# Kernel tuning notes

Hardware: AMD Instinct MI355X
Metric: run time of the kernel (lower is better)

## Reference

```python
import jax, jax.numpy as jnp
import numpy as np

NUM_HEADS = 16

def setup_inputs() -> dict:
    key = jax.random.key(0)
    ks = jax.random.split(key, 7)
    B, N, D = 2, 2048, 1024
    x = jax.random.normal(ks[0], (B, N, D), dtype=jnp.float32)
    gamma = jax.random.uniform(ks[1], (B, NUM_HEADS), dtype=jnp.float32)
    dist_matrix = jax.random.uniform(ks[2], (N, N), dtype=jnp.float32)
    W_qkv = jax.random.normal(ks[3], (D, 3 * D), dtype=jnp.float32) * (D ** -0.5)
    b_qkv = jnp.zeros((3 * D,), dtype=jnp.float32)
    W_proj = jax.random.normal(ks[4], (D, D), dtype=jnp.float32) * (D ** -0.5)
    b_proj = jnp.zeros((D,), dtype=jnp.float32)
    return {"x": x, "gamma": gamma, "dist_matrix": dist_matrix,
            "W_qkv": W_qkv, "b_qkv": b_qkv, "W_proj": W_proj, "b_proj": b_proj}

def reference(x, gamma, dist_matrix, W_qkv, b_qkv, W_proj, b_proj):
    B, N, D = x.shape
    H = NUM_HEADS
    hd = D // H
    scale = D ** -0.5  # standard_scale=False -> dim**-0.5
    # qkv projection: [B,N,3D] -> [3,B,H,N,hd]
    qkv = (x @ W_qkv + b_qkv).reshape(B, N, 3, H, hd).transpose(2, 0, 3, 1, 4)
    q, k, v = qkv[0], qkv[1], qkv[2]
    # scores with zoom bias: [B,H,N,N]
    scores = jnp.einsum('bhnd,bhmd->bhnm', q, k) * scale
    scores = scores - gamma[:, :, None, None] * dist_matrix[None, None, :, :]
    attn = jax.nn.softmax(scores, axis=-1)
    out = jnp.einsum('bhnm,bhmd->bhnd', attn, v)  # [B,H,N,hd]
    out = out.transpose(0, 2, 1, 3).reshape(B, N, D)
    return out @ W_proj + b_proj
```

## Files before the change

kernel.cpp:

```cpp
#include <hip/hip_runtime.h>
#include <cstdint>
#include <cstddef>

#define HD 64
#define NH 16
#define BATCH 2
#define SEQ 2048
#define DIM 1024
#define SCALE 0.03125f
#define LOG2E 1.4426950408889634f
#define QSCALE (SCALE * LOG2E)
#define NT (SEQ / 64)
#define NT2 32
#define SOFF 16.0f

typedef short bf16x8 __attribute__((ext_vector_type(8)));
typedef float f32x4 __attribute__((ext_vector_type(4)));
typedef unsigned u32x2 __attribute__((ext_vector_type(2)));
typedef unsigned u32x4 __attribute__((ext_vector_type(4)));

#define GL16(gp, lp) __builtin_amdgcn_global_load_lds( \
    (const __attribute__((address_space(1))) unsigned int*)(gp), \
    (__attribute__((address_space(3))) unsigned int*)(lp), 16, 0, 0)

static __device__ __forceinline__ unsigned short f2bf(float f) {
  union { float f; unsigned u; } a; a.f = f;
  unsigned r = a.u + 0x7fffu + ((a.u >> 16) & 1u);
  return (unsigned short)(r >> 16);
}

static __device__ __forceinline__ f32x4 zero4() {
  f32x4 z; z[0] = 0.f; z[1] = 0.f; z[2] = 0.f; z[3] = 0.f; return z;
}

__global__ void convert_x(const float* __restrict__ in, unsigned short* __restrict__ out, int n4) {
  int i = blockIdx.x * blockDim.x + threadIdx.x;
  if (i < n4) {
    float4 v = reinterpret_cast<const float4*>(in)[i];
    ushort4 o;
    o.x = f2bf(v.x); o.y = f2bf(v.y); o.z = f2bf(v.z); o.w = f2bf(v.w);
    reinterpret_cast<ushort4*>(out)[i] = o;
  }
}

__global__ void transpose_convert(const float* __restrict__ in, unsigned short* __restrict__ out,
                                  int R, int C) {
  __shared__ float tile[32][33];
  int bx = blockIdx.x * 32;
  int by = blockIdx.y * 32;
  int tx = threadIdx.x, ty = threadIdx.y;
  #pragma unroll
  for (int i = 0; i < 32; i += 8)
    tile[ty + i][tx] = in[(size_t)(by + ty + i) * C + bx + tx];
  __syncthreads();
  #pragma unroll
  for (int i = 0; i < 32; i += 8)
    out[(size_t)(bx + ty + i) * R + by + tx] = f2bf(tile[tx][ty + i]);
}

__global__ __launch_bounds__(256) void gemm128(
    const unsigned short* __restrict__ A, const unsigned short* __restrict__ Bt,
    const float* __restrict__ bias, int K, int mode,
    unsigned short* __restrict__ qo, unsigned short* __restrict__ ko,
    unsigned short* __restrict__ vo, float* __restrict__ outf) {
  __shared__ __attribute__((aligned(16))) unsigned short As[128 * 64];
  __shared__ __attribute__((aligned(16))) unsigned short Bs[128 * 64];
  const int tid = threadIdx.x;
  const int lane = tid & 63, w = tid >> 6;
  const int lo = lane & 15, hi = lane >> 4;
  const int wm = w >> 1, wn = w & 1;
  const int gx = gridDim.x;
  const int nwg = gx * gridDim.y;
  const int flat = blockIdx.y * gx + blockIdx.x;
  const int swz = (flat & 7) * (nwg >> 3) + (flat >> 3);
  const int m0 = (swz / gx) * 128, n0 = (swz % gx) * 128;
  const int srow = tid >> 3, scol = (tid & 7) * 8;
  const unsigned short* abase = A + (size_t)(m0 + srow) * K + scol;
  const unsigned short* bbase = Bt + (size_t)(n0 + srow) * K + scol;

  f32x4 acc[4][4];
  #pragma unroll
  for (int mr = 0; mr < 4; ++mr)
    #pragma unroll
    for (int nr = 0; nr < 4; ++nr) acc[mr][nr] = zero4();

  const int nkt = K / 64;
  for (int kt = 0; kt < nkt; ++kt) {
    const unsigned short* ak = abase + kt * 64;
    const unsigned short* bk = bbase + kt * 64;
    #pragma unroll
    for (int i = 0; i < 4; ++i) {
      GL16(ak + (size_t)(32 * i) * K, &As[(w * 64 + 256 * i) * 8]);
      GL16(bk + (size_t)(32 * i) * K, &Bs[(w * 64 + 256 * i) * 8]);
    }
    __syncthreads();
    __builtin_amdgcn_s_setprio(1);
    #pragma unroll
    for (int kc = 0; kc < 2; ++kc) {
      bf16x8 af[4], bfr[4];
      #pragma unroll
      for (int mr = 0; mr < 4; ++mr)
        af[mr] = *reinterpret_cast<const bf16x8*>(
            &As[(wm * 64 + mr * 16 + lo) * 64 + kc * 32 + hi * 8]);
      #pragma unroll
      for (int nr = 0; nr < 4; ++nr)
        bfr[nr] = *reinterpret_cast<const bf16x8*>(
            &Bs[(wn * 64 + nr * 16 + lo) * 64 + kc * 32 + hi * 8]);
      #pragma unroll
      for (int mr = 0; mr < 4; ++mr)
        #pragma unroll
        for (int nr = 0; nr < 4; ++nr)
          acc[mr][nr] = __builtin_amdgcn_mfma_f32_16x16x32_bf16(af[mr], bfr[nr], acc[mr][nr], 0, 0, 0);
    }
    __builtin_amdgcn_s_setprio(0);
    __syncthreads();
  }

  #pragma unroll
  for (int nr = 0; nr < 4; ++nr) {
    const int gcol = n0 + wn * 64 + nr * 16 + lo;
    const float bv = bias[gcol];
    #pragma unroll
    for (int mr = 0; mr < 4; ++mr)
      #pragma unroll
      for (int j = 0; j < 4; ++j) {
        const int grow = m0 + wm * 64 + mr * 16 + hi * 4 + j;
        float val = acc[mr][nr][j] + bv;
        if (mode == 0) {
          int which = gcol >> 10;
          int hh = (gcol >> 6) & 15;
          int d = gcol & 63;
          int bb = grow >> 11;
          int n = grow & 2047;
          if (which == 0) {
            qo[((size_t)(bb * NH + hh) * SEQ + n) * HD + d] = f2bf(val * QSCALE);
          } else if (which == 1) {
            ko[((size_t)(bb * NH + hh) * SEQ + n) * HD + d] = f2bf(val);
          } else {
            vo[((size_t)(bb * NH + hh) * HD + d) * SEQ + n] = f2bf(val);
          }
        } else {
          outf[(size_t)grow * DIM + gcol] = val;
        }
      }
  }
}

__global__ __launch_bounds__(256, 6) void attn_split(
    const unsigned short* __restrict__ qb, const unsigned short* __restrict__ kb,
    const unsigned short* __restrict__ vtb, const float* __restrict__ gamma,
    const float* __restrict__ dist, float* __restrict__ oP, float* __restrict__ lP) {
  __shared__ __attribute__((aligned(16))) unsigned short Ks[2][32 * 64];
  __shared__ __attribute__((aligned(16))) unsigned short Vt[2][64 * 32];
  __shared__ __attribute__((aligned(16))) unsigned short Ps[4 * 16 * 32];
  const int tid = threadIdx.x;
  const int lane = tid & 63;
  const int w = tid >> 6;
  const int lo = lane & 15;
  const int hi = lane >> 4;
  const int idx = blockIdx.x;
  const int half = idx & 1;
  const int bh = (idx >> 1) & 31;
  const int qt = idx >> 6;
  const int qrow0 = qt * 64 + w * 16;
  const int kv0 = half * 1024;
  const float g2 = gamma[bh] * LOG2E;

  const size_t base = (size_t)bh * SEQ * HD;
  const size_t vtbase = (size_t)bh * HD * SEQ;

  bf16x8 qf[2];
  #pragma unroll
  for (int kc = 0; kc < 2; ++kc)
    qf[kc] = *reinterpret_cast<const bf16x8*>(
        &qb[base + (size_t)(qrow0 + lo) * HD + kc * 32 + hi * 8]);

  const float* drow = dist + (size_t)(qrow0 + lo) * SEQ + kv0 + hi * 4;

  f32x4 o[4];
  #pragma unroll
  for (int db = 0; db < 4; ++db) o[db] = zero4();
  float l_run = 0.f;

  const int ksr = tid >> 3;
  const int ksc = (tid & 7) ^ (ksr & 7);
  const unsigned short* ksrc = kb + base + (size_t)(kv0 + ksr) * HD + ksc * 8;
  const int vsr = tid >> 2;
  const int vsc = (tid & 3) ^ ((vsr >> 1) & 3);
  const unsigned short* vsrc = vtb + vtbase + (size_t)vsr * SEQ + kv0 + vsc * 8;

  unsigned short* const psw = &Ps[w * 512 + lo * 32];

  GL16(ksrc, &Ks[0][w * 512]);
  GL16(vsrc, &Vt[0][w * 512]);

#define SITER(T, CUR)                                                                  \
  {                                                                                    \
                                              \
    asm volatile("s_waitcnt vmcnt(1)" ::: "memory");                                   \
    __builtin_amdgcn_s_barrier();                                                      \
          \
    f32x4 dv[2];                                                                       \
    { const float* dp = drow + (T) * 32;                                               \
      dv[0] = *reinterpret_cast<const f32x4*>(dp);                                     \
      dv[1] = *reinterpret_cast<const f32x4*>(dp + 16);                                \
    }                                                                                  \
    __builtin_amdgcn_sched_barrier(0);                                                 \
    if ((T) + 1 < NT2) {                                                               \
      GL16(ksrc + (size_t)((T) + 1) * 32 * HD, &Ks[(CUR) ^ 1][w * 512]);               \
    }                                                                                  \
    __builtin_amdgcn_sched_barrier(0);                                                 \
                                                            \
    f32x4 s[2];                                                                        \
    s[0][0] = -SOFF; s[0][1] = -SOFF; s[0][2] = -SOFF; s[0][3] = -SOFF;                \
    s[1] = s[0];                                                                       \
    __builtin_amdgcn_s_setprio(1);                                                     \
    _Pragma("unroll")                                                                  \
    for (int nb = 0; nb < 2; ++nb)                                                     \
      _Pragma("unroll")                                                                \
      for (int kc = 0; kc < 2; ++kc) {                                                 \
        bf16x8 kf = *reinterpret_cast<const bf16x8*>(                                  \
            &Ks[CUR][(nb * 16 + lo) * 64 + ((kc * 4 + hi) ^ (lo & 7)) * 8]);           \
        s[nb] = __builtin_amdgcn_mfma_f32_16x16x32_bf16(kf, qf[kc], s[nb], 0, 0, 0);   \
      }                                                                                \
    __builtin_amdgcn_s_setprio(0);                                                     \
                \
    float psum = 0.f;                                                                  \
    _Pragma("unroll")                                                                  \
    for (int nb = 0; nb < 2; ++nb) {                                                   \
      float p0 = exp2f(__builtin_fmaf(-g2, dv[nb][0], s[nb][0]));                      \
      float p1 = exp2f(__builtin_fmaf(-g2, dv[nb][1], s[nb][1]));                      \
      float p2 = exp2f(__builtin_fmaf(-g2, dv[nb][2], s[nb][2]));                      \
      float p3 = exp2f(__builtin_fmaf(-g2, dv[nb][3], s[nb][3]));                      \
      psum += (p0 + p1) + (p2 + p3);                                                   \
      unsigned pk0, pk1;                                                               \
      asm("v_cvt_pk_bf16_f32 %0, %1, %2" : "=v"(pk0) : "v"(p0), "v"(p1));              \
      asm("v_cvt_pk_bf16_f32 %0, %1, %2" : "=v"(pk1) : "v"(p2), "v"(p3));              \
      u32x2 pw_; pw_[0] = pk0; pw_[1] = pk1;                                           \
      *reinterpret_cast<u32x2*>(&psw[((nb * 4 + hi) ^ (lo & 7)) * 4]) = pw_;           \
    }                                                                                  \
    psum += __shfl_xor(psum, 16, 64);                                                  \
    psum += __shfl_xor(psum, 32, 64);                                                  \
    l_run += psum;                                                                     \
                                  \
    if ((T) + 1 < NT2)                                                                 \
      asm volatile("s_waitcnt vmcnt(1)" ::: "memory");                                 \
    else                                                                               \
      asm volatile("s_waitcnt vmcnt(0)" ::: "memory");                                 \
    __builtin_amdgcn_s_barrier();                                                      \
    if ((T) + 1 < NT2) {                                                               \
      GL16(vsrc + ((T) + 1) * 32, &Vt[(CUR) ^ 1][w * 512]);                            \
    }                                                                                  \
    __builtin_amdgcn_sched_barrier(0);                                                 \
                                               \
    __builtin_amdgcn_s_setprio(1);                                                     \
    {                                                                                  \
      u32x2 ra = *reinterpret_cast<const u32x2*>(&psw[((hi * 2) ^ (lo & 7)) * 4]);     \
      u32x2 rb = *reinterpret_cast<const u32x2*>(&psw[((hi * 2 + 1) ^ (lo & 7)) * 4]); \
      u32x4 t_; t_[0] = ra[0]; t_[1] = ra[1]; t_[2] = rb[0]; t_[3] = rb[1];            \
      bf16x8 pf = __builtin_bit_cast(bf16x8, t_);                                      \
      _Pragma("unroll")                                                                \
      for (int db = 0; db < 4; ++db) {                                                 \
        bf16x8 vtf = *reinterpret_cast<const bf16x8*>(                                 \
            &Vt[CUR][(db * 16 + lo) * 32 + ((hi ^ ((lo >> 1) & 3))) * 8]);             \
        o[db] = __builtin_amdgcn_mfma_f32_16x16x32_bf16(vtf, pf, o[db], 0, 0, 0);      \
      }                                                                                \
    }                                                                                  \
    __builtin_amdgcn_s_setprio(0);                                                     \
  }

  for (int mt = 0; mt < NT2; mt += 2) {
    SITER(mt, 0)
    SITER(mt + 1, 1)
  }
#undef SITER

  {
    const size_t prow = (size_t)(half * 32 + bh) * SEQ + qrow0 + lo;
    float* op = oP + prow * HD + hi * 4;
    #pragma unroll
    for (int db = 0; db < 4; ++db)
      *reinterpret_cast<f32x4*>(op + db * 16) = o[db];
    if (hi == 0) lP[prow] = l_run;
  }
}

__global__ __launch_bounds__(256) void attn_combine(
    const float* __restrict__ oP, const float* __restrict__ lP,
    unsigned short* __restrict__ ab) {
  int g = blockIdx.x * blockDim.x + threadIdx.x;
  int row = g >> 4;
  int dc = (g & 15) * 4;
  int bh = row >> 11, n = row & 2047;
  int b = bh >> 4, h = bh & 15;
  f32x4 a = *reinterpret_cast<const f32x4*>(oP + (size_t)row * 64 + dc);
  f32x4 c = *reinterpret_cast<const f32x4*>(oP + 4194304 + (size_t)row * 64 + dc);
  float rl = 1.0f / (lP[row] + lP[65536 + row]);
  ushort4 w4;
  w4.x = f2bf((a[0] + c[0]) * rl);
  w4.y = f2bf((a[1] + c[1]) * rl);
  w4.z = f2bf((a[2] + c[2]) * rl);
  w4.w = f2bf((a[3] + c[3]) * rl);
  *reinterpret_cast<ushort4*>(&ab[((size_t)(b * SEQ + n)) * DIM + h * HD + dc]) = w4;
}

__global__ __launch_bounds__(256, 4) void attn_kernel(
    const unsigned short* __restrict__ qb, const unsigned short* __restrict__ kb,
    const unsigned short* __restrict__ vtb, const float* __restrict__ gamma,
    const float* __restrict__ dist, unsigned short* __restrict__ ab) {
  __shared__ __attribute__((aligned(16))) unsigned short Ks[2][64 * 64];
  __shared__ __attribute__((aligned(16))) unsigned short Vt[2][64 * 64];
  __shared__ __attribute__((aligned(16))) unsigned short Ps[4 * 16 * 64];
  const int tid = threadIdx.x;
  const int lane = tid & 63;
  const int w = tid >> 6;
  const int lo = lane & 15;
  const int hi = lane >> 4;
  const int idx = blockIdx.x;
  const int bh = idx & 31;
  const int qt = idx >> 5;
  const int b = bh >> 4, h = bh & 15;
  const int qrow0 = qt * 64 + w * 16;
  const float g2 = gamma[bh] * LOG2E;

  const size_t base = (size_t)bh * SEQ * HD;
  const size_t vtbase = (size_t)bh * HD * SEQ;

  bf16x8 qf[2];
  #pragma unroll
  for (int kc = 0; kc < 2; ++kc)
    qf[kc] = *reinterpret_cast<const bf16x8*>(
        &qb[base + (size_t)(qrow0 + lo) * HD + kc * 32 + hi * 8]);

  const float* drow = dist + (size_t)(qrow0 + lo) * SEQ + hi * 4;

  f32x4 o[4];
  #pragma unroll
  for (int db = 0; db < 4; ++db) o[db] = zero4();
  float l_run = 0.f;

  const int srow = tid >> 3;
  const int schunk = (tid & 7) ^ (srow & 7);
  const unsigned short* ksrc0 = kb + base + (size_t)srow * HD + schunk * 8;
  const unsigned short* ksrc1 = ksrc0 + (size_t)32 * HD;
  const unsigned short* vsrc0 = vtb + vtbase + (size_t)srow * SEQ + schunk * 8;
  const unsigned short* vsrc1 = vsrc0 + (size_t)32 * SEQ;

  unsigned short* const psw = &Ps[w * 1024 + lo * 64];

  GL16(ksrc0, &Ks[0][w * 512]);
  GL16(ksrc1, &Ks[0][2048 + w * 512]);
  GL16(vsrc0, &Vt[0][w * 512]);
  GL16(vsrc1, &Vt[0][2048 + w * 512]);

#define ITER(T, CUR)                                                                   \
  {                                                                                    \
    asm volatile("s_waitcnt vmcnt(2)" ::: "memory");                                   \
    __builtin_amdgcn_s_barrier();                                                      \
    f32x4 dv[4];                                                                       \
    { const float* dp = drow + (T) * 64;                                               \
      _Pragma("unroll")                                                                \
      for (int nb = 0; nb < 4; ++nb)                                                   \
        dv[nb] = *reinterpret_cast<const f32x4*>(dp + nb * 16);                        \
    }                                                                                  \
    __builtin_amdgcn_sched_barrier(0);                                                 \
    if ((T) + 1 < NT) {                                                                \
      const size_t m1 = (size_t)((T) + 1) * 64;                                        \
      GL16(ksrc0 + m1 * HD, &Ks[(CUR) ^ 1][w * 512]);                                  \
      GL16(ksrc1 + m1 * HD, &Ks[(CUR) ^ 1][2048 + w * 512]);                           \
    }                                                                                  \
    __builtin_amdgcn_sched_barrier(0);                                                 \
    f32x4 s[4];                                                                        \
    _Pragma("unroll")                                                                  \
    for (int nb = 0; nb < 4; ++nb) {                                                   \
      s[nb][0] = -SOFF; s[nb][1] = -SOFF; s[nb][2] = -SOFF; s[nb][3] = -SOFF;          \
    }                                                                                  \
    __builtin_amdgcn_s_setprio(1);                                                     \
    _Pragma("unroll")                                                                  \
    for (int nb = 0; nb < 4; ++nb)                                                     \
      _Pragma("unroll")                                                                \
      for (int kc = 0; kc < 2; ++kc) {                                                 \
        bf16x8 kf = *reinterpret_cast<const bf16x8*>(                                  \
            &Ks[CUR][(nb * 16 + lo) * 64 + ((kc * 4 + hi) ^ (lo & 7)) * 8]);           \
        s[nb] = __builtin_amdgcn_mfma_f32_16x16x32_bf16(kf, qf[kc], s[nb], 0, 0, 0);   \
      }                                                                                \
    __builtin_amdgcn_s_setprio(0);                                                     \
    float psum = 0.f;                                                                  \
    _Pragma("unroll")                                                                  \
    for (int nb = 0; nb < 4; ++nb) {                                                   \
      float p0 = exp2f(__builtin_fmaf(-g2, dv[nb][0], s[nb][0]));                      \
      float p1 = exp2f(__builtin_fmaf(-g2, dv[nb][1], s[nb][1]));                      \
      float p2 = exp2f(__builtin_fmaf(-g2, dv[nb][2], s[nb][2]));                      \
      float p3 = exp2f(__builtin_fmaf(-g2, dv[nb][3], s[nb][3]));                      \
      psum += (p0 + p1) + (p2 + p3);                                                   \
      unsigned pk0, pk1;                                                               \
      asm("v_cvt_pk_bf16_f32 %0, %1, %2" : "=v"(pk0) : "v"(p0), "v"(p1));              \
      asm("v_cvt_pk_bf16_f32 %0, %1, %2" : "=v"(pk1) : "v"(p2), "v"(p3));              \
      u32x2 pw_; pw_[0] = pk0; pw_[1] = pk1;                                           \
      *reinterpret_cast<u32x2*>(&psw[(((nb << 2) + hi) ^ lo) * 4]) = pw_;              \
    }                                                                                  \
    psum += __shfl_xor(psum, 16, 64);                                                  \
    psum += __shfl_xor(psum, 32, 64);                                                  \
    l_run += psum;                                                                     \
    if ((T) + 1 < NT)                                                                  \
      asm volatile("s_waitcnt vmcnt(2)" ::: "memory");                                 \
    else                                                                               \
      asm volatile("s_waitcnt vmcnt(0)" ::: "memory");                                 \
    __builtin_amdgcn_s_barrier();                                                      \
    if ((T) + 1 < NT) {                                                                \
      const int m1 = ((T) + 1) * 64;                                                   \
      GL16(vsrc0 + m1, &Vt[(CUR) ^ 1][w * 512]);                                       \
      GL16(vsrc1 + m1, &Vt[(CUR) ^ 1][2048 + w * 512]);                                \
    }                                                                                  \
    __builtin_amdgcn_sched_barrier(0);                                                 \
    __builtin_amdgcn_s_setprio(1);                                                     \
    _Pragma("unroll")                                                                  \
    for (int kc = 0; kc < 2; ++kc) {                                                   \
      u32x2 ra = *reinterpret_cast<const u32x2*>(&psw[(((kc << 3) + hi * 2) ^ lo) * 4]); \
      u32x2 rb = *reinterpret_cast<const u32x2*>(&psw[(((kc << 3) + hi * 2 + 1) ^ lo) * 4]); \
      u32x4 t_; t_[0] = ra[0]; t_[1] = ra[1]; t_[2] = rb[0]; t_[3] = rb[1];            \
      bf16x8 pf = __builtin_bit_cast(bf16x8, t_);                                      \
      _Pragma("unroll")                                                                \
      for (int db = 0; db < 4; ++db) {                                                 \
        bf16x8 vtf = *reinterpret_cast<const bf16x8*>(                                 \
            &Vt[CUR][(db * 16 + lo) * 64 + ((kc * 4 + hi) ^ (lo & 7)) * 8]);           \
        o[db] = __builtin_amdgcn_mfma_f32_16x16x32_bf16(vtf, pf, o[db], 0, 0, 0);      \
      }                                                                                \
    }                                                                                  \
    __builtin_amdgcn_s_setprio(0);                                                     \
  }

  for (int mt = 0; mt < NT; mt += 2) {
    ITER(mt, 0)
    ITER(mt + 1, 1)
  }
#undef ITER

  {
    float rl = 1.0f / l_run;
    size_t row = (size_t)b * SEQ + qrow0 + lo;
    #pragma unroll
    for (int db = 0; db < 4; ++db) {
      ushort4 w4;
      w4.x = f2bf(o[db][0] * rl);
      w4.y = f2bf(o[db][1] * rl);
      w4.z = f2bf(o[db][2] * rl);
      w4.w = f2bf(o[db][3] * rl);
      *reinterpret_cast<ushort4*>(&ab[row * DIM + h * HD + db * 16 + hi * 4]) = w4;
    }
  }
}

extern "C" void kernel_launch(void* const* d_in, const int* in_sizes, int n_in,
                              void* d_out, int out_size, void* d_ws, size_t ws_size,
                              hipStream_t stream) {
  const float* x     = (const float*)d_in[0];
  const float* gamma = (const float*)d_in[1];
  const float* dist  = (const float*)d_in[2];
  const float* Wqkv  = (const float*)d_in[3];
  const float* bqkv  = (const float*)d_in[4];
  const float* Wproj = (const float*)d_in[5];
  const float* bproj = (const float*)d_in[6];
  float* out = (float*)d_out;

  char* ws = (char*)d_ws;
  unsigned short* xb     = (unsigned short*)(ws);
  unsigned short* wqkvt  = (unsigned short*)(ws + 8388608);
  unsigned short* wprojt = (unsigned short*)(ws + 14680064);
  unsigned short* qbuf   = (unsigned short*)(ws + 16777216);
  unsigned short* kbuf   = (unsigned short*)(ws + 25165824);
  unsigned short* vtbuf  = (unsigned short*)(ws + 33554432);
  unsigned short* abuf   = (unsigned short*)(ws + 41943040);
  float* oP = (float*)(ws + 50331648);
  float* lP = (float*)(ws + 83886080);
  const bool split = ws_size >= (size_t)84410368;

  convert_x<<<4096, 256, 0, stream>>>(x, xb, (BATCH * SEQ * DIM) / 4);
  transpose_convert<<<dim3(96, 32), dim3(32, 8), 0, stream>>>(Wqkv, wqkvt, DIM, 3 * DIM);
  transpose_convert<<<dim3(32, 32), dim3(32, 8), 0, stream>>>(Wproj, wprojt, DIM, DIM);
  gemm128<<<dim3(24, 32), 256, 0, stream>>>(xb, wqkvt, bqkv, DIM, 0, qbuf, kbuf, vtbuf, nullptr);
  if (split) {
    attn_split<<<2048, 256, 0, stream>>>(qbuf, kbuf, vtbuf, gamma, dist, oP, lP);
    attn_combine<<<4096, 256, 0, stream>>>(oP, lP, abuf);
  } else {
    attn_kernel<<<(SEQ / 64) * BATCH * NH, 256, 0, stream>>>(qbuf, kbuf, vtbuf, gamma, dist, abuf);
  }
  gemm128<<<dim3(8, 32), 256, 0, stream>>>(abuf, wprojt, bproj, DIM, 1, nullptr, nullptr, nullptr, out);
}
```

Measured before the change: 192.5 us.

## Rework split attention to 32x32 MFMA tiles with register-level P transpose

Rewrites the split-KV attention kernel to use 32x32x16 bf16 MFMAs, with each wave owning 32 query rows and each block covering 128 query rows over 64-key tiles. The probability matrix is rearranged between the S and PV MFMAs with v_permlane32_swap in registers, replacing the previous round trip through an LDS scratch buffer. This cuts LDS traffic and per-MFMA overhead and halves the block count. The cost is higher register pressure (launch bounds lowered to 2), bigger K/V LDS tiles, and fewer blocks to spread across the CUs.

```diff
diff --git a/kernel.cpp b/kernel.cpp
--- a/kernel.cpp
+++ b/kernel.cpp
@@ -11,11 +11,12 @@
 #define LOG2E 1.4426950408889634f
 #define QSCALE (SCALE * LOG2E)
 #define NT (SEQ / 64)
-#define NT2 32
+#define NTH 16
 #define SOFF 16.0f
 
 typedef short bf16x8 __attribute__((ext_vector_type(8)));
 typedef float f32x4 __attribute__((ext_vector_type(4)));
+typedef float f32x16 __attribute__((ext_vector_type(16)));
 typedef unsigned u32x2 __attribute__((ext_vector_type(2)));
 typedef unsigned u32x4 __attribute__((ext_vector_type(4)));
 
@@ -146,142 +147,165 @@
   }
 }
 
-__global__ __launch_bounds__(256, 6) void attn_split(
+__global__ __launch_bounds__(256, 2) void attn_split2(
     const unsigned short* __restrict__ qb, const unsigned short* __restrict__ kb,
     const unsigned short* __restrict__ vtb, const float* __restrict__ gamma,
     const float* __restrict__ dist, float* __restrict__ oP, float* __restrict__ lP) {
-  __shared__ __attribute__((aligned(16))) unsigned short Ks[2][32 * 64];
-  __shared__ __attribute__((aligned(16))) unsigned short Vt[2][64 * 32];
-  __shared__ __attribute__((aligned(16))) unsigned short Ps[4 * 16 * 32];
+  __shared__ __attribute__((aligned(16))) unsigned short Ks[2][64 * 64];
+  __shared__ __attribute__((aligned(16))) unsigned short Vt[2][64 * 64];
   const int tid = threadIdx.x;
   const int lane = tid & 63;
   const int w = tid >> 6;
-  const int lo = lane & 15;
-  const int hi = lane >> 4;
+  const int q5 = lane & 31;
+  const int h5 = lane >> 5;
   const int idx = blockIdx.x;
   const int half = idx & 1;
   const int bh = (idx >> 1) & 31;
   const int qt = idx >> 6;
-  const int qrow0 = qt * 64 + w * 16;
+  const int qrow0 = qt * 128 + w * 32;
   const int kv0 = half * 1024;
   const float g2 = gamma[bh] * LOG2E;
 
   const size_t base = (size_t)bh * SEQ * HD;
   const size_t vtbase = (size_t)bh * HD * SEQ;
 
-  bf16x8 qf[2];
-  #pragma unroll
-  for (int kc = 0; kc < 2; ++kc)
-    qf[kc] = *reinterpret_cast<const bf16x8*>(
-        &qb[base + (size_t)(qrow0 + lo) * HD + kc * 32 + hi * 8]);
-
-  const float* drow = dist + (size_t)(qrow0 + lo) * SEQ + kv0 + hi * 4;
-
-  f32x4 o[4];
-  #pragma unroll
-  for (int db = 0; db < 4; ++db) o[db] = zero4();
+  bf16x8 qf[4];
+  #pragma unroll
+  for (int ks = 0; ks < 4; ++ks)
+    qf[ks] = *reinterpret_cast<const bf16x8*>(
+        &qb[base + (size_t)(qrow0 + q5) * HD + ks * 16 + h5 * 8]);
+
+  const float* drow = dist + (size_t)(qrow0 + q5) * SEQ + kv0 + 4 * h5;
+
+  f32x16 o[2];
+  #pragma unroll
+  for (int i = 0; i < 16; ++i) { o[0][i] = 0.f; o[1][i] = 0.f; }
   float l_run = 0.f;
 
-  const int ksr = tid >> 3;
-  const int ksc = (tid & 7) ^ (ksr & 7);
-  const unsigned short* ksrc = kb + base + (size_t)(kv0 + ksr) * HD + ksc * 8;
-  const int vsr = tid >> 2;
-  const int vsc = (tid & 3) ^ ((vsr >> 1) & 3);
-  const unsigned short* vsrc = vtb + vtbase + (size_t)vsr * SEQ + kv0 + vsc * 8;
-
-  unsigned short* const psw = &Ps[w * 512 + lo * 32];
-
-  GL16(ksrc, &Ks[0][w * 512]);
-  GL16(vsrc, &Vt[0][w * 512]);
+  const int srow = tid >> 3;
+  const int schunk = (tid & 7) ^ (srow & 7);
+  const unsigned short* ksrc0 = kb + base + (size_t)(kv0 + srow) * HD + schunk * 8;
+  const unsigned short* ksrc1 = ksrc0 + (size_t)32 * HD;
+  const unsigned short* vsrc0 = vtb + vtbase + (size_t)srow * SEQ + kv0 + schunk * 8;
+  const unsigned short* vsrc1 = vsrc0 + (size_t)32 * SEQ;
+
+  GL16(ksrc0, &Ks[0][w * 512]);
+  GL16(ksrc1, &Ks[0][2048 + w * 512]);
+  GL16(vsrc0, &Vt[0][w * 512]);
+  GL16(vsrc1, &Vt[0][2048 + w * 512]);
 
 #define SITER(T, CUR)                                                                  \
   {                                                                                    \
-                                              \
-    asm volatile("s_waitcnt vmcnt(1)" ::: "memory");                                   \
+                                   \
+    asm volatile("s_waitcnt vmcnt(2)" ::: "memory");                                   \
     __builtin_amdgcn_s_barrier();                                                      \
-          \
-    f32x4 dv[2];                                                                       \
-    { const float* dp = drow + (T) * 32;                                               \
-      dv[0] = *reinterpret_cast<const f32x4*>(dp);                                     \
-      dv[1] = *reinterpret_cast<const f32x4*>(dp + 16);                                \
+       \
+    f32x4 dv[2][4];                                                                    \
+    { const float* dp = drow + (T) * 64;                                               \
+      _Pragma("unroll")                                                                \
+      for (int blk = 0; blk < 2; ++blk)                                                \
+        _Pragma("unroll")                                                              \
+        for (int rp = 0; rp < 4; ++rp)                                                 \
+          dv[blk][rp] = *reinterpret_cast<const f32x4*>(dp + 32 * blk + 8 * rp);       \
     }                                                                                  \
     __builtin_amdgcn_sched_barrier(0);                                                 \
-    if ((T) + 1 < NT2) {                                                               \
-      GL16(ksrc + (size_t)((T) + 1) * 32 * HD, &Ks[(CUR) ^ 1][w * 512]);               \
+    if ((T) + 1 < NTH) {                                                               \
+      const size_t m1 = (size_t)((T) + 1) * 64;                                        \
+      GL16(ksrc0 + m1 * HD, &Ks[(CUR) ^ 1][w * 512]);                                  \
+      GL16(ksrc1 + m1 * HD, &Ks[(CUR) ^ 1][2048 + w * 512]);                           \
     }                                                                                  \
     __builtin_amdgcn_sched_barrier(0);                                                 \
-                                                            \
-    f32x4 s[2];                                                                        \
-    s[0][0] = -SOFF; s[0][1] = -SOFF; s[0][2] = -SOFF; s[0][3] = -SOFF;                \
-    s[1] = s[0];                                                                       \
+                     \
+    f32x16 s[2];                                                                       \
+    _Pragma("unroll")                                                                  \
+    for (int i = 0; i < 16; ++i) { s[0][i] = -SOFF; s[1][i] = -SOFF; }                 \
     __builtin_amdgcn_s_setprio(1);                                                     \
     _Pragma("unroll")                                                                  \
-    for (int nb = 0; nb < 2; ++nb)                                                     \
-      _Pragma("unroll")                                                                \
-      for (int kc = 0; kc < 2; ++kc) {                                                 \
+    for (int blk = 0; blk < 2; ++blk)                                                  \
+      _Pragma("unroll")                                                                \
+      for (int ks = 0; ks < 4; ++ks) {                                                 \
         bf16x8 kf = *reinterpret_cast<const bf16x8*>(                                  \
-            &Ks[CUR][(nb * 16 + lo) * 64 + ((kc * 4 + hi) ^ (lo & 7)) * 8]);           \
-        s[nb] = __builtin_amdgcn_mfma_f32_16x16x32_bf16(kf, qf[kc], s[nb], 0, 0, 0);   \
+            &Ks[CUR][(blk * 32 + q5) * 64 + ((ks * 2 + h5) ^ (q5 & 7)) * 8]);          \
+        s[blk] = __builtin_amdgcn_mfma_f32_32x32x16_bf16(kf, qf[ks], s[blk], 0, 0, 0); \
       }                                                                                \
     __builtin_amdgcn_s_setprio(0);                                                     \
-                \
+                           \
     float psum = 0.f;                                                                  \
-    _Pragma("unroll")                                                                  \
-    for (int nb = 0; nb < 2; ++nb) {                                                   \
-      float p0 = exp2f(__builtin_fmaf(-g2, dv[nb][0], s[nb][0]));                      \
-      float p1 = exp2f(__builtin_fmaf(-g2, dv[nb][1], s[nb][1]));                      \
-      float p2 = exp2f(__builtin_fmaf(-g2, dv[nb][2], s[nb][2]));                      \
-      float p3 = exp2f(__builtin_fmaf(-g2, dv[nb][3], s[nb][3]));                      \
-      psum += (p0 + p1) + (p2 + p3);                                                   \
-      unsigned pk0, pk1;                                                               \
-      asm("v_cvt_pk_bf16_f32 %0, %1, %2" : "=v"(pk0) : "v"(p0), "v"(p1));              \
-      asm("v_cvt_pk_bf16_f32 %0, %1, %2" : "=v"(pk1) : "v"(p2), "v"(p3));              \
-      u32x2 pw_; pw_[0] = pk0; pw_[1] = pk1;                                           \
-      *reinterpret_cast<u32x2*>(&psw[((nb * 4 + hi) ^ (lo & 7)) * 4]) = pw_;           \
-    }                                                                                  \
-    psum += __shfl_xor(psum, 16, 64);                                                  \
+    unsigned u[2][4][2];                                                               \
+    _Pragma("unroll")                                                                  \
+    for (int blk = 0; blk < 2; ++blk)                                                  \
+      _Pragma("unroll")                                                                \
+      for (int rp = 0; rp < 4; ++rp) {                                                 \
+        float p0 = exp2f(__builtin_fmaf(-g2, dv[blk][rp][0], s[blk][rp * 4 + 0]));     \
+        float p1 = exp2f(__builtin_fmaf(-g2, dv[blk][rp][1], s[blk][rp * 4 + 1]));     \
+        float p2 = exp2f(__builtin_fmaf(-g2, dv[blk][rp][2], s[blk][rp * 4 + 2]));     \
+        float p3 = exp2f(__builtin_fmaf(-g2, dv[blk][rp][3], s[blk][rp * 4 + 3]));     \
+        psum += (p0 + p1) + (p2 + p3);                                                 \
+        asm("v_cvt_pk_bf16_f32 %0, %1, %2" : "=v"(u[blk][rp][0]) : "v"(p0), "v"(p1));  \
+        asm("v_cvt_pk_bf16_f32 %0, %1, %2" : "=v"(u[blk][rp][1]) : "v"(p2), "v"(p3));  \
+      }                                                                                \
     psum += __shfl_xor(psum, 32, 64);                                                  \
     l_run += psum;                                                                     \
-                                  \
-    if ((T) + 1 < NT2)                                                                 \
-      asm volatile("s_waitcnt vmcnt(1)" ::: "memory");                                 \
+            \
+    unsigned pu[4][4];                                                                 \
+    _Pragma("unroll")                                                                  \
+    for (int blk = 0; blk < 2; ++blk)                                                  \
+      _Pragma("unroll")                                                                \
+      for (int jp = 0; jp < 2; ++jp) {                                                 \
+        unsigned a0 = u[blk][0][jp], b0 = u[blk][1][jp];                               \
+        asm("v_permlane32_swap_b32 %0, %1" : "+v"(a0), "+v"(b0));                      \
+        pu[2 * blk][jp] = a0; pu[2 * blk][2 + jp] = b0;                                \
+        unsigned a1 = u[blk][2][jp], b1 = u[blk][3][jp];                               \
+        asm("v_permlane32_swap_b32 %0, %1" : "+v"(a1), "+v"(b1));                      \
+        pu[2 * blk + 1][jp] = a1; pu[2 * blk + 1][2 + jp] = b1;                        \
+      }                                                                                \
+           \
+    if ((T) + 1 < NTH)                                                                 \
+      asm volatile("s_waitcnt vmcnt(2)" ::: "memory");                                 \
     else                                                                               \
       asm volatile("s_waitcnt vmcnt(0)" ::: "memory");                                 \
     __builtin_amdgcn_s_barrier();                                                      \
-    if ((T) + 1 < NT2) {                                                               \
-      GL16(vsrc + ((T) + 1) * 32, &Vt[(CUR) ^ 1][w * 512]);                            \
+    if ((T) + 1 < NTH) {                                                               \
+      const int m1 = ((T) + 1) * 64;                                                   \
+      GL16(vsrc0 + m1, &Vt[(CUR) ^ 1][w * 512]);                                       \
+      GL16(vsrc1 + m1, &Vt[(CUR) ^ 1][2048 + w * 512]);                                \
     }                                                                                  \
     __builtin_amdgcn_sched_barrier(0);                                                 \
-                                               \
+                                         \
     __builtin_amdgcn_s_setprio(1);                                                     \
-    {                                                                                  \
-      u32x2 ra = *reinterpret_cast<const u32x2*>(&psw[((hi * 2) ^ (lo & 7)) * 4]);     \
-      u32x2 rb = *reinterpret_cast<const u32x2*>(&psw[((hi * 2 + 1) ^ (lo & 7)) * 4]); \
-      u32x4 t_; t_[0] = ra[0]; t_[1] = ra[1]; t_[2] = rb[0]; t_[3] = rb[1];            \
+    _Pragma("unroll")                                                                  \
+    for (int ks = 0; ks < 4; ++ks) {                                                   \
+      u32x4 t_; t_[0] = pu[ks][0]; t_[1] = pu[ks][1]; t_[2] = pu[ks][2]; t_[3] = pu[ks][3]; \
       bf16x8 pf = __builtin_bit_cast(bf16x8, t_);                                      \
       _Pragma("unroll")                                                                \
-      for (int db = 0; db < 4; ++db) {                                                 \
+      for (int db = 0; db < 2; ++db) {                                                 \
         bf16x8 vtf = *reinterpret_cast<const bf16x8*>(                                 \
-            &Vt[CUR][(db * 16 + lo) * 32 + ((hi ^ ((lo >> 1) & 3))) * 8]);             \
-        o[db] = __builtin_amdgcn_mfma_f32_16x16x32_bf16(vtf, pf, o[db], 0, 0, 0);      \
+            &Vt[CUR][(db * 32 + q5) * 64 + ((ks * 2 + h5) ^ (q5 & 7)) * 8]);           \
+        o[db] = __builtin_amdgcn_mfma_f32_32x32x16_bf16(vtf, pf, o[db], 0, 0, 0);      \
       }                                                                                \
     }                                                                                  \
     __builtin_amdgcn_s_setprio(0);                                                     \
   }
 
-  for (int mt = 0; mt < NT2; mt += 2) {
+  for (int mt = 0; mt < NTH; mt += 2) {
     SITER(mt, 0)
     SITER(mt + 1, 1)
   }
 #undef SITER
 
   {
-    const size_t prow = (size_t)(half * 32 + bh) * SEQ + qrow0 + lo;
-    float* op = oP + prow * HD + hi * 4;
+    const size_t prow = (size_t)(half * 32 + bh) * SEQ + qrow0 + q5;
+    float* op = oP + prow * HD + 4 * h5;
     #pragma unroll
-    for (int db = 0; db < 4; ++db)
-      *reinterpret_cast<f32x4*>(op + db * 16) = o[db];
-    if (hi == 0) lP[prow] = l_run;
+    for (int db = 0; db < 2; ++db)
+      #pragma unroll
+      for (int rp = 0; rp < 4; ++rp) {
+        f32x4 t;
+        t[0] = o[db][rp * 4 + 0]; t[1] = o[db][rp * 4 + 1];
+        t[2] = o[db][rp * 4 + 2]; t[3] = o[db][rp * 4 + 3];
+        *reinterpret_cast<f32x4*>(op + db * 32 + 8 * rp) = t;
+      }
+    if (h5 == 0) lP[prow] = l_run;
   }
 }
 
@@ -480,7 +504,7 @@
   transpose_convert<<<dim3(32, 32), dim3(32, 8), 0, stream>>>(Wproj, wprojt, DIM, DIM);
   gemm128<<<dim3(24, 32), 256, 0, stream>>>(xb, wqkvt, bqkv, DIM, 0, qbuf, kbuf, vtbuf, nullptr);
   if (split) {
-    attn_split<<<2048, 256, 0, stream>>>(qbuf, kbuf, vtbuf, gamma, dist, oP, lP);
+    attn_split2<<<1024, 256, 0, stream>>>(qbuf, kbuf, vtbuf, gamma, dist, oP, lP);
     attn_combine<<<4096, 256, 0, stream>>>(oP, lP, abuf);
   } else {
     attn_kernel<<<(SEQ / 64) * BATCH * NH, 256, 0, stream>>>(qbuf, kbuf, vtbuf, gamma, dist, abuf);
```

Result: no change. 193.6 us (+0.6%).
